# Optimization experiments

Hardware: AMD Instinct MI355X
Metric: run time of the kernel (lower is better)

## Reference

```python
import jax, jax.numpy as jnp
import numpy as np

B, N, D, H = 4, 4096, 1024, 16
DH = D // H          # per-head dim = 64
M = 256              # number of random features
KEPS = 1e-3          # performer kernel epsilon
LNEPS = 1e-5


def setup_inputs() -> dict:
    key = jax.random.key(0)
    ks = jax.random.split(key, 16)
    s = 0.02
    return {
        "src": jax.random.normal(ks[0], (B, N, D), jnp.float32),
        "Wq": s * jax.random.normal(ks[1], (D, D), jnp.float32),
        "Wk": s * jax.random.normal(ks[2], (D, D), jnp.float32),
        "Wv": s * jax.random.normal(ks[3], (D, D), jnp.float32),
        "Wout": s * jax.random.normal(ks[4], (D, D), jnp.float32),
        "b_out": jnp.zeros((D,), jnp.float32),
        "proj": jax.random.normal(ks[5], (M, DH), jnp.float32),
        "g1": jnp.ones((D,), jnp.float32),
        "beta1": jnp.zeros((D,), jnp.float32),
        "W1": s * jax.random.normal(ks[6], (2048, D), jnp.float32),
        "b1": jnp.zeros((2048,), jnp.float32),
        "W2": s * jax.random.normal(ks[7], (D, 2048), jnp.float32),
        "b2": jnp.zeros((D,), jnp.float32),
        "g2": jnp.ones((D,), jnp.float32),
        "beta2": jnp.zeros((D,), jnp.float32),
    }


def _layernorm(x, g, b):
    mu = x.mean(-1, keepdims=True)
    var = ((x - mu) ** 2).mean(-1, keepdims=True)
    return (x - mu) * jax.lax.rsqrt(var + LNEPS) * g + b


def _softmax_kernel(x, proj, is_query):
    # FAVOR+ positive softmax kernel feature map (performer_pytorch)
    dn = DH ** -0.25           # data normalizer d^{-1/4}
    ratio = M ** -0.5
    data_dash = jnp.einsum('bhnd,md->bhnm', x * dn, proj)
    diag = (x ** 2).sum(-1) * 0.5 * dn * dn            # [b,h,n]
    if is_query:
        stab = data_dash.max(-1, keepdims=True)
    else:
        stab = data_dash.max()
    return ratio * (jnp.exp(data_dash - diag[..., None] - stab) + KEPS)


def reference(src, Wq, Wk, Wv, Wout, b_out, proj, g1, beta1, W1, b1, W2, b2, g2, beta2):
    # ---- Performer self-attention (FAVOR+, non-causal) ----
    def split_heads(x):
        return x.reshape(B, N, H, DH).transpose(0, 2, 1, 3)  # [b,h,n,dh]

    q = split_heads(src @ Wq.T)
    k = split_heads(src @ Wk.T)
    v = split_heads(src @ Wv.T)

    qp = _softmax_kernel(q, proj, is_query=True)   # [b,h,n,m]
    kp = _softmax_kernel(k, proj, is_query=False)  # [b,h,n,m]

    k_sum = kp.sum(-2)                                        # [b,h,m]
    d_inv = 1.0 / jnp.einsum('bhnm,bhm->bhn', qp, k_sum)      # [b,h,n]
    context = jnp.einsum('bhnm,bhnd->bhmd', kp, v)            # [b,h,m,dh]
    attn = jnp.einsum('bhnm,bhmd->bhnd', qp, context) * d_inv[..., None]

    attn = attn.transpose(0, 2, 1, 3).reshape(B, N, D)
    src2 = attn @ Wout.T + b_out

    # ---- residual + norm + FFN (dropout = identity at eval) ----
    x = _layernorm(src + src2, g1, beta1)
    ff = (jax.nn.gelu(x @ W1.T + b1, approximate=False)) @ W2.T + b2
    return _layernorm(x + ff, g2, beta2)
```

## Files before the change

kernel.cpp:

```cpp
#include <hip/hip_runtime.h>

#define DEVI __device__ __forceinline__

using u16 = unsigned short;
using u32 = unsigned int;
using u64 = unsigned long long;

typedef __bf16 bf16x8 __attribute__((ext_vector_type(8)));
typedef __bf16 bf16x4 __attribute__((ext_vector_type(4)));
typedef float  f32x4  __attribute__((ext_vector_type(4)));

constexpr int BB = 4, NN = 4096, DD = 1024, HH = 16, DH = 64, MF = 256;
constexpr int RT = BB * NN;
constexpr int QKVS = 3072;
constexpr float DN    = 0.35355339059327373f;
constexpr float RATIO = 0.0625f;
constexpr float DIAGC = 0.0625f;
constexpr float KEPSC = 1e-3f;

DEVI u16 f2bf(float f) {
  u32 u = __float_as_uint(f);
  u32 r = u + 0x7fffu + ((u >> 16) & 1u);
  return (u16)(r >> 16);
}
DEVI float bf2f(u16 u) { return __uint_as_float(((u32)u) << 16); }

typedef void __attribute__((address_space(1)))* gas1;
typedef void __attribute__((address_space(3)))* las3;
DEVI void gload_lds16(const void* g, void* l) {
  __builtin_amdgcn_global_load_lds((gas1)(u64)g, (las3)(u32)(u64)l, 16, 0, 0);
}

DEVI bf16x8 ldswz(const u16* base, int row, int kbyte) {
  int p = (row << 7) + kbyte;
  p ^= (row & 7) << 4;
  return *(const bf16x8*)((const char*)base + p);
}

__global__ void cast_kernel(const float* __restrict__ in, u16* __restrict__ out, int n4) {
  int i = blockIdx.x * 256 + threadIdx.x;
  int stride = gridDim.x * 256;
  for (; i < n4; i += stride) {
    float4 v = ((const float4*)in)[i];
    ushort4 o; o.x = f2bf(v.x); o.y = f2bf(v.y); o.z = f2bf(v.z); o.w = f2bf(v.w);
    ((ushort4*)out)[i] = o;
  }
}

__global__ void cast_weights_kernel(
    const float* __restrict__ Wq, const float* __restrict__ Wk,
    const float* __restrict__ Wv, const float* __restrict__ Wout,
    const float* __restrict__ W1, const float* __restrict__ W2,
    const float* __restrict__ proj,
    u16* __restrict__ wqkvb, u16* __restrict__ wob,
    u16* __restrict__ w1b, u16* __restrict__ w2b, u16* __restrict__ projb)
{
  constexpr int TOT = 2101248;
  int i = blockIdx.x * 256 + threadIdx.x;
  const int stride = gridDim.x * 256;
  for (; i < TOT; i += stride) {
    const float* s; u16* d; int loc; float sc = 1.0f;
    if (i < 1048576) {
      int seg = i >> 18; loc = i & 262143;
      s = (seg == 0) ? Wq : (seg == 1) ? Wk : (seg == 2) ? Wv : Wout;
      d = (seg < 3) ? (wqkvb + seg * 1048576) : wob;
    } else if (i < 1572864) { loc = i - 1048576; s = W1; d = w1b; }
    else if (i < 2097152)   { loc = i - 1572864; s = W2; d = w2b; }
    else                    { loc = i - 2097152; s = proj; d = projb; sc = DN; }
    float4 v = ((const float4*)s)[loc];
    ushort4 o; o.x = f2bf(v.x * sc); o.y = f2bf(v.y * sc); o.z = f2bf(v.z * sc); o.w = f2bf(v.w * sc);
    ((ushort4*)d)[loc] = o;
  }
}

template <int EPI>
__global__ __launch_bounds__(256, 2) void gemm_bt(
    const u16* __restrict__ A, int lda, const u16* __restrict__ Bm,
    u16* __restrict__ Cb, const float* __restrict__ bias,
    int Ncols, int K)
{
  __shared__ __align__(16) u16 sA[128 * 64];
  __shared__ __align__(16) u16 sB[128 * 64];
  const int tid = threadIdx.x, lane = tid & 63;
  const int wv = tid >> 6, wr = wv >> 1, wc = wv & 1;

  const int gx = gridDim.x;
  const int wg = blockIdx.y * gx + blockIdx.x;
  const int cpx = (gx * gridDim.y) >> 3;
  const int swz = (wg & 7) * cpx + (wg >> 3);
  const int bn = swz % gx, bm = swz / gx;

  f32x4 acc[4][4] = {};

  int rowS[4], colS[4], ldsb[4];
#pragma unroll
  for (int it = 0; it < 4; ++it) {
    int p = (it * 256 + tid) * 16;
    ldsb[it] = (it * 256 + (tid & ~63)) * 16;
    int sp = p ^ (((p >> 7) & 7) << 4);
    rowS[it] = sp >> 7;
    colS[it] = (sp >> 1) & 63;
  }
  const size_t baseA = (size_t)bm * 128, baseB = (size_t)bn * 128;

  for (int kt = 0; kt < K; kt += 64) {
#pragma unroll
    for (int it = 0; it < 4; ++it)
      gload_lds16(A + (baseA + rowS[it]) * lda + kt + colS[it], (char*)sA + ldsb[it]);
#pragma unroll
    for (int it = 0; it < 4; ++it)
      gload_lds16(Bm + (baseB + rowS[it]) * K + kt + colS[it], (char*)sB + ldsb[it]);
    __syncthreads();
#pragma unroll
    for (int kk = 0; kk < 2; ++kk) {
      const int kbyte = kk * 64 + ((lane >> 4) << 4);
      bf16x8 a[4], b[4];
#pragma unroll
      for (int i = 0; i < 4; ++i) a[i] = ldswz(sA, wr * 64 + i * 16 + (lane & 15), kbyte);
#pragma unroll
      for (int i = 0; i < 4; ++i) b[i] = ldswz(sB, wc * 64 + i * 16 + (lane & 15), kbyte);
#pragma unroll
      for (int i = 0; i < 4; ++i)
#pragma unroll
        for (int j = 0; j < 4; ++j)
          acc[i][j] = __builtin_amdgcn_mfma_f32_16x16x32_bf16(a[i], b[j], acc[i][j], 0, 0, 0);
    }
    __syncthreads();
  }

#pragma unroll
  for (int i = 0; i < 4; ++i) {
    const int gr0 = bm * 128 + wr * 64 + i * 16 + ((lane >> 4) << 2);
#pragma unroll
    for (int j = 0; j < 4; ++j) {
      const int gc = bn * 128 + wc * 64 + j * 16 + (lane & 15);
#pragma unroll
      for (int r = 0; r < 4; ++r) {
        const size_t o = (size_t)(gr0 + r) * Ncols + gc;
        const float v = acc[i][j][r];
        if constexpr (EPI == 0) {
          Cb[o] = f2bf(v);
        } else if constexpr (EPI == 2) {
          float t = v + bias[gc];
          Cb[o] = f2bf(0.5f * t * (1.0f + erff(t * 0.70710678118654752f)));
        } else {
          Cb[o] = f2bf(v + bias[gc]);
        }
      }
    }
  }
}

__global__ __launch_bounds__(256) void kmax_kernel(
    const u16* __restrict__ qkvb, const u16* __restrict__ projb, float* __restrict__ pmax)
{
  __shared__ __align__(16) u16 sX[64 * 72];
  __shared__ float sred[4];
  const int tid = threadIdx.x, lane = tid & 63, wv = tid >> 6;
  const int bh = blockIdx.x, b = bh >> 4, h = bh & 15;
  const int n0 = blockIdx.y * 64;

  for (int i = tid; i < 512; i += 256) {
    int r = i >> 3, c8 = (i & 7) << 3;
    uint4 v = *(const uint4*)(qkvb + ((size_t)(b * NN + n0 + r)) * QKVS + 1024 + h * DH + c8);
    *(uint4*)&sX[r * 72 + c8] = v;
  }
  __syncthreads();

  f32x4 dacc[16] = {};
#pragma unroll
  for (int kk = 0; kk < 2; ++kk) {
    const int ko = kk * 32 + ((lane >> 4) << 3);
    bf16x8 a = *(const bf16x8*)&sX[(wv * 16 + (lane & 15)) * 72 + ko];
#pragma unroll
    for (int f = 0; f < 16; ++f) {
      bf16x8 bb = *(const bf16x8*)(projb + (f * 16 + (lane & 15)) * 64 + ko);
      dacc[f] = __builtin_amdgcn_mfma_f32_16x16x32_bf16(a, bb, dacc[f], 0, 0, 0);
    }
  }
  float mx = -1e30f;
#pragma unroll
  for (int f = 0; f < 16; ++f)
#pragma unroll
    for (int r = 0; r < 4; ++r) mx = fmaxf(mx, dacc[f][r]);
#pragma unroll
  for (int m = 1; m < 64; m <<= 1) mx = fmaxf(mx, __shfl_xor(mx, m));
  if (lane == 0) sred[wv] = mx;
  __syncthreads();
  if (tid == 0)
    pmax[blockIdx.y * gridDim.x + blockIdx.x] =
        fmaxf(fmaxf(sred[0], sred[1]), fmaxf(sred[2], sred[3]));
}

__global__ __launch_bounds__(256) void reduce_max_kernel(
    const float* __restrict__ pmax, float* __restrict__ stab)
{
  const int tid = threadIdx.x;
  float mx = -1e30f;
#pragma unroll
  for (int i = 0; i < 16; ++i) mx = fmaxf(mx, pmax[i * 256 + tid]);
#pragma unroll
  for (int m = 1; m < 64; m <<= 1) mx = fmaxf(mx, __shfl_xor(mx, m));
  __shared__ float sred[4];
  if ((tid & 63) == 0) sred[tid >> 6] = mx;
  __syncthreads();
  if (tid == 0)
    stab[0] = fmaxf(fmaxf(sred[0], sred[1]), fmaxf(sred[2], sred[3]));
}

__global__ __launch_bounds__(512, 4) void kctx_kernel(
    const u16* __restrict__ qkvb, const u16* __restrict__ projb,
    const float* __restrict__ stab_p,
    float* __restrict__ ctxP, float* __restrict__ ksum)
{
  __shared__ __align__(16) u16 sX[64 * 72];
  __shared__ __align__(16) u16 sVT[64 * 68];
  __shared__ __align__(16) u16 sKpT[256 * 72];
  __shared__ float sDiag[64];
  const int tid = threadIdx.x, lane = tid & 63, wv = tid >> 6;
  const int nw = wv & 3;
  const int mh = wv >> 2;
  const int bh = blockIdx.x, b = bh >> 4, h = bh & 15;
  const int sl = blockIdx.y;
  const float stab = stab_p[0];

  f32x4 cacc[8] = {};
  float ksacc[8] = {};
  const int row_base = nw * 16 + ((lane >> 4) << 2);

  for (int t = 0; t < 8; ++t) {
    const int n0 = sl * 512 + t * 64;
    if (t) __syncthreads();
    {
      int r = tid >> 3, c8 = (tid & 7) << 3;
      size_t g = ((size_t)(b * NN + n0 + r)) * QKVS + h * DH + c8;
      uint4 xv = *(const uint4*)(qkvb + g + 1024);
      *(uint4*)&sX[r * 72 + c8] = xv;
      {
        const u16* px = (const u16*)&xv;
        float s = 0;
#pragma unroll
        for (int j = 0; j < 8; ++j) { float x = bf2f(px[j]); s += x * x; }
        s += __shfl_xor(s, 1); s += __shfl_xor(s, 2); s += __shfl_xor(s, 4);
        if ((tid & 7) == 0) sDiag[r] = DIAGC * s;
      }
      uint4 vv = *(const uint4*)(qkvb + g + 2048);
      const u16* pv = (const u16*)&vv;
#pragma unroll
      for (int j = 0; j < 8; ++j) sVT[(c8 + j) * 68 + r] = pv[j];
    }
    __syncthreads();

    f32x4 dacc[8] = {};
#pragma unroll
    for (int kk = 0; kk < 2; ++kk) {
      const int ko = kk * 32 + ((lane >> 4) << 3);
      bf16x8 a = *(const bf16x8*)&sX[(nw * 16 + (lane & 15)) * 72 + ko];
#pragma unroll
      for (int f = 0; f < 8; ++f) {
        bf16x8 bb = *(const bf16x8*)(projb + (mh * 128 + f * 16 + (lane & 15)) * 64 + ko);
        dacc[f] = __builtin_amdgcn_mfma_f32_16x16x32_bf16(a, bb, dacc[f], 0, 0, 0);
      }
    }
#pragma unroll
    for (int f = 0; f < 8; ++f) {
      float kvv[4]; float cs = 0;
#pragma unroll
      for (int r = 0; r < 4; ++r) {
        float val = RATIO * (__expf(dacc[f][r] - sDiag[row_base + r] - stab) + KEPSC);
        kvv[r] = val; cs += val;
      }
      cs += __shfl_xor(cs, 16); cs += __shfl_xor(cs, 32);
      ksacc[f] += cs;
      ushort4 pk; pk.x = f2bf(kvv[0]); pk.y = f2bf(kvv[1]); pk.z = f2bf(kvv[2]); pk.w = f2bf(kvv[3]);
      *(ushort4*)&sKpT[(mh * 128 + f * 16 + (lane & 15)) * 72 + row_base] = pk;
    }
    __syncthreads();
#pragma unroll
    for (int kk = 0; kk < 2; ++kk) {
      const int ko = kk * 32 + ((lane >> 4) << 3);
      const int vrow = nw * 16 + (lane & 15);
      bf16x4 lo = *(const bf16x4*)&sVT[vrow * 68 + ko];
      bf16x4 hi = *(const bf16x4*)&sVT[vrow * 68 + ko + 4];
      bf16x8 a;
#pragma unroll
      for (int e = 0; e < 4; ++e) { a[e] = lo[e]; a[e + 4] = hi[e]; }
#pragma unroll
      for (int f = 0; f < 8; ++f) {
        bf16x8 bb = *(const bf16x8*)&sKpT[(mh * 128 + f * 16 + (lane & 15)) * 72 + ko];
        cacc[f] = __builtin_amdgcn_mfma_f32_16x16x32_bf16(a, bb, cacc[f], 0, 0, 0);
      }
    }
  }
  float* cp = ctxP + (size_t)(sl * 64 + bh) * 16384;
#pragma unroll
  for (int f = 0; f < 8; ++f) {
    const int m = mh * 128 + f * 16 + (lane & 15);
#pragma unroll
    for (int r = 0; r < 4; ++r)
      cp[(row_base + r) * 256 + m] = cacc[f][r];
  }
  if (lane < 16) {
#pragma unroll
    for (int f = 0; f < 8; ++f)
      atomicAdd(&ksum[bh * 256 + mh * 128 + f * 16 + lane], ksacc[f]);
  }
}

__global__ __launch_bounds__(256) void ctxfin_kernel(
    const float* __restrict__ ctxP, u16* __restrict__ ctxb)
{
  const int idx = blockIdx.x * 256 + threadIdx.x;
  const int bh = idx >> 12, pos = idx & 4095;
  float4 s = {0, 0, 0, 0};
#pragma unroll
  for (int sl = 0; sl < 8; ++sl) {
    float4 v = *(const float4*)(ctxP + (size_t)(sl * 64 + bh) * 16384 + pos * 4);
    s.x += v.x; s.y += v.y; s.z += v.z; s.w += v.w;
  }
  ushort4 o; o.x = f2bf(s.x); o.y = f2bf(s.y); o.z = f2bf(s.z); o.w = f2bf(s.w);
  *(ushort4*)(ctxb + (size_t)bh * 16384 + pos * 4) = o;
}

__global__ __launch_bounds__(256, 2) void qattn_kernel(
    u16* qkvb, const u16* __restrict__ projb,
    const u16* __restrict__ ctxb, const float* __restrict__ ksum)
{
  __shared__ __align__(16) u16 sCtx[64 * 256];
  __shared__ __align__(16) u16 sX[64 * 72];
  __shared__ __align__(16) u16 sQp[64 * 264];
  __shared__ float sKsum[256];
  __shared__ float sDiag[64];
  __shared__ float sDinv[64];
  const int tid = threadIdx.x, lane = tid & 63, wv = tid >> 6;
  const int bh = blockIdx.x, b = bh >> 4, h = bh & 15;

  {
    const char* cbase = (const char*)(ctxb + (size_t)bh * 16384);
#pragma unroll
    for (int it = 0; it < 8; ++it) {
      int p = (it * 256 + tid) * 16;
      int ldsb = (it * 256 + (tid & ~63)) * 16;
      int q = p ^ (((p >> 9) & 7) << 4);
      gload_lds16(cbase + q, (char*)sCtx + ldsb);
    }
  }
  sKsum[tid] = ksum[bh * 256 + tid];

  const int row_base = wv * 16 + ((lane >> 4) << 2);
  const int wr = wv >> 1, wc = wv & 1;

  for (int rt = 0; rt < 2; ++rt) {
    const int n0 = (blockIdx.y * 2 + rt) * 64;
    for (int i = tid; i < 512; i += 256) {
      int r = i >> 3, c8 = (i & 7) << 3;
      uint4 v = *(const uint4*)(qkvb + ((size_t)(b * NN + n0 + r)) * QKVS + h * DH + c8);
      *(uint4*)&sX[r * 72 + c8] = v;
    }
    __syncthreads();
    {
      int r = tid >> 2, qq = tid & 3;
      float s = 0;
#pragma unroll
      for (int j = 0; j < 16; ++j) { float x = bf2f(sX[r * 72 + qq * 16 + j]); s += x * x; }
      s += __shfl_xor(s, 1); s += __shfl_xor(s, 2);
      if (qq == 0) sDiag[r] = DIAGC * s;
    }
    f32x4 dacc[16] = {};
#pragma unroll
    for (int kk = 0; kk < 2; ++kk) {
      const int ko = kk * 32 + ((lane >> 4) << 3);
      bf16x8 a = *(const bf16x8*)&sX[(wv * 16 + (lane & 15)) * 72 + ko];
#pragma unroll
      for (int f = 0; f < 16; ++f) {
        bf16x8 bb = *(const bf16x8*)(projb + (f * 16 + (lane & 15)) * 64 + ko);
        dacc[f] = __builtin_amdgcn_mfma_f32_16x16x32_bf16(a, bb, dacc[f], 0, 0, 0);
      }
    }
    __syncthreads();
#pragma unroll
    for (int r = 0; r < 4; ++r) {
      const int row = row_base + r;
      float mx = dacc[0][r];
#pragma unroll
      for (int f = 1; f < 16; ++f) mx = fmaxf(mx, dacc[f][r]);
      mx = fmaxf(mx, __shfl_xor(mx, 1));
      mx = fmaxf(mx, __shfl_xor(mx, 2));
      mx = fmaxf(mx, __shfl_xor(mx, 4));
      mx = fmaxf(mx, __shfl_xor(mx, 8));
      const float dg = sDiag[row];
      float ds = 0;
#pragma unroll
      for (int f = 0; f < 16; ++f) {
        float qv = RATIO * (__expf(dacc[f][r] - dg - mx) + KEPSC);
        dacc[f][r] = qv;
        ds += qv * sKsum[f * 16 + (lane & 15)];
      }
      ds += __shfl_xor(ds, 1); ds += __shfl_xor(ds, 2);
      ds += __shfl_xor(ds, 4); ds += __shfl_xor(ds, 8);
      if ((lane & 15) == 0) sDinv[row] = 1.0f / ds;
    }
#pragma unroll
    for (int f = 0; f < 16; ++f)
#pragma unroll
      for (int r = 0; r < 4; ++r)
        sQp[(row_base + r) * 264 + f * 16 + (lane & 15)] = f2bf(dacc[f][r]);
    __syncthreads();

    f32x4 acc2[2][2] = {};
#pragma unroll
    for (int kk = 0; kk < 8; ++kk) {
      const int koe = kk * 32 + ((lane >> 4) << 3);
      const int kob = koe * 2;
      bf16x8 a0 = *(const bf16x8*)&sQp[(wr * 32 + (lane & 15)) * 264 + koe];
      bf16x8 a1 = *(const bf16x8*)&sQp[(wr * 32 + 16 + (lane & 15)) * 264 + koe];
      const int j0 = wc * 32 + (lane & 15), j1 = j0 + 16;
      bf16x8 b0 = *(const bf16x8*)((const char*)sCtx + (((j0 << 9) + kob) ^ ((j0 & 7) << 4)));
      bf16x8 b1 = *(const bf16x8*)((const char*)sCtx + (((j1 << 9) + kob) ^ ((j1 & 7) << 4)));
      acc2[0][0] = __builtin_amdgcn_mfma_f32_16x16x32_bf16(a0, b0, acc2[0][0], 0, 0, 0);
      acc2[0][1] = __builtin_amdgcn_mfma_f32_16x16x32_bf16(a0, b1, acc2[0][1], 0, 0, 0);
      acc2[1][0] = __builtin_amdgcn_mfma_f32_16x16x32_bf16(a1, b0, acc2[1][0], 0, 0, 0);
      acc2[1][1] = __builtin_amdgcn_mfma_f32_16x16x32_bf16(a1, b1, acc2[1][1], 0, 0, 0);
    }
#pragma unroll
    for (int mi = 0; mi < 2; ++mi)
#pragma unroll
      for (int ni = 0; ni < 2; ++ni)
#pragma unroll
        for (int r = 0; r < 4; ++r) {
          const int row = wr * 32 + mi * 16 + ((lane >> 4) << 2) + r;
          const int col = wc * 32 + ni * 16 + (lane & 15);
          float v = acc2[mi][ni][r] * sDinv[row];
          qkvb[((size_t)(b * NN + n0 + row)) * QKVS + h * DH + col] = f2bf(v);
        }
    __syncthreads();
  }
}

__global__ __launch_bounds__(256) void ln1_kernel(
    const float* __restrict__ src, const u16* __restrict__ wout,
    const float* __restrict__ g, const float* __restrict__ be, u16* __restrict__ xb)
{
  const int row = blockIdx.x, tid = threadIdx.x;
  const float4 sv = ((const float4*)(src + (size_t)row * DD))[tid];
  const ushort4 wv = ((const ushort4*)(wout + (size_t)row * DD))[tid];
  float x0 = sv.x + bf2f(wv.x);
  float x1 = sv.y + bf2f(wv.y);
  float x2 = sv.z + bf2f(wv.z);
  float x3 = sv.w + bf2f(wv.w);
  float s = x0 + x1 + x2 + x3;
  float ss = x0 * x0 + x1 * x1 + x2 * x2 + x3 * x3;
#pragma unroll
  for (int m = 1; m < 64; m <<= 1) { s += __shfl_xor(s, m); ss += __shfl_xor(ss, m); }
  __shared__ float red[8];
  if ((tid & 63) == 0) { red[tid >> 6] = s; red[4 + (tid >> 6)] = ss; }
  __syncthreads();
  s = red[0] + red[1] + red[2] + red[3];
  ss = red[4] + red[5] + red[6] + red[7];
  const float mu = s * (1.0f / DD);
  const float rs = rsqrtf(ss * (1.0f / DD) - mu * mu + 1e-5f);
  const float4 gv = ((const float4*)g)[tid];
  const float4 bv = ((const float4*)be)[tid];
  ushort4 o;
  o.x = f2bf((x0 - mu) * rs * gv.x + bv.x);
  o.y = f2bf((x1 - mu) * rs * gv.y + bv.y);
  o.z = f2bf((x2 - mu) * rs * gv.z + bv.z);
  o.w = f2bf((x3 - mu) * rs * gv.w + bv.w);
  ((ushort4*)(xb + (size_t)row * DD))[tid] = o;
}

__global__ __launch_bounds__(256) void ln2_kernel(
    const u16* __restrict__ xb, const u16* __restrict__ ff,
    const float* __restrict__ g, const float* __restrict__ be, float* __restrict__ out)
{
  const int row = blockIdx.x, tid = threadIdx.x;
  const ushort4 xv = ((const ushort4*)(xb + (size_t)row * DD))[tid];
  const ushort4 fv = ((const ushort4*)(ff + (size_t)row * DD))[tid];
  float x0 = bf2f(xv.x) + bf2f(fv.x);
  float x1 = bf2f(xv.y) + bf2f(fv.y);
  float x2 = bf2f(xv.z) + bf2f(fv.z);
  float x3 = bf2f(xv.w) + bf2f(fv.w);
  float s = x0 + x1 + x2 + x3;
  float ss = x0 * x0 + x1 * x1 + x2 * x2 + x3 * x3;
#pragma unroll
  for (int m = 1; m < 64; m <<= 1) { s += __shfl_xor(s, m); ss += __shfl_xor(ss, m); }
  __shared__ float red[8];
  if ((tid & 63) == 0) { red[tid >> 6] = s; red[4 + (tid >> 6)] = ss; }
  __syncthreads();
  s = red[0] + red[1] + red[2] + red[3];
  ss = red[4] + red[5] + red[6] + red[7];
  const float mu = s * (1.0f / DD);
  const float rs = rsqrtf(ss * (1.0f / DD) - mu * mu + 1e-5f);
  const float4 gv = ((const float4*)g)[tid];
  const float4 bv = ((const float4*)be)[tid];
  float4 o;
  o.x = (x0 - mu) * rs * gv.x + bv.x;
  o.y = (x1 - mu) * rs * gv.y + bv.y;
  o.z = (x2 - mu) * rs * gv.z + bv.z;
  o.w = (x3 - mu) * rs * gv.w + bv.w;
  ((float4*)(out + (size_t)row * DD))[tid] = o;
}

extern "C" void kernel_launch(void* const* d_in, const int* in_sizes, int n_in,
                              void* d_out, int out_size, void* d_ws, size_t ws_size,
                              hipStream_t stream) {
  (void)in_sizes; (void)n_in; (void)out_size; (void)ws_size;
  const float* src   = (const float*)d_in[0];
  const float* Wq    = (const float*)d_in[1];
  const float* Wk    = (const float*)d_in[2];
  const float* Wv    = (const float*)d_in[3];
  const float* Wout  = (const float*)d_in[4];
  const float* b_out = (const float*)d_in[5];
  const float* proj  = (const float*)d_in[6];
  const float* g1    = (const float*)d_in[7];
  const float* be1   = (const float*)d_in[8];
  const float* W1    = (const float*)d_in[9];
  const float* b1    = (const float*)d_in[10];
  const float* W2    = (const float*)d_in[11];
  const float* b2    = (const float*)d_in[12];
  const float* g2    = (const float*)d_in[13];
  const float* be2   = (const float*)d_in[14];

  char* ws = (char*)d_ws;
  constexpr size_t OFF_SRCB = 0;
  constexpr size_t OFF_QKV  = 33554432;
  constexpr size_t OFF_XB   = 67108864;
  constexpr size_t OFF_WOUTB= 100663296;
  constexpr size_t OFF_WQKV = 134217728;
  constexpr size_t OFF_WO   = 140509184;
  constexpr size_t OFF_W1   = 142606336;
  constexpr size_t OFF_W2   = 146800640;
  constexpr size_t OFF_PROJ = 150994944;
  constexpr size_t OFF_CTXB = 151027712;
  constexpr size_t OFF_KSUM = 153124864;
  constexpr size_t OFF_PMAX = 153190400;
  constexpr size_t OFF_STAB = 153206784;

  u16* srcb  = (u16*)(ws + OFF_SRCB);
  u16* qkvb  = (u16*)(ws + OFF_QKV);
  u16* wqkvb = (u16*)(ws + OFF_WQKV);
  u16* wob   = (u16*)(ws + OFF_WO);
  u16* w1b   = (u16*)(ws + OFF_W1);
  u16* w2b   = (u16*)(ws + OFF_W2);
  u16* projb = (u16*)(ws + OFF_PROJ);
  u16* ctxb  = (u16*)(ws + OFF_CTXB);
  float* ksum = (float*)(ws + OFF_KSUM);
  float* pmax = (float*)(ws + OFF_PMAX);
  float* stab = (float*)(ws + OFF_STAB);
  float* ctxP = (float*)(ws + OFF_SRCB);
  u16* woutb = (u16*)(ws + OFF_WOUTB);
  u16* xb    = (u16*)(ws + OFF_XB);
  u16* h1    = (u16*)(ws + OFF_SRCB);
  u16* ff    = (u16*)(ws + OFF_WOUTB);

  cast_kernel<<<4096, 256, 0, stream>>>(src, srcb, RT * DD / 4);
  cast_weights_kernel<<<2048, 256, 0, stream>>>(Wq, Wk, Wv, Wout, W1, W2, proj,
                                                wqkvb, wob, w1b, w2b, projb);
  hipMemsetAsync(ws + OFF_KSUM, 0, 65536, stream);

  gemm_bt<0><<<dim3(QKVS / 128, RT / 128), 256, 0, stream>>>(srcb, DD, wqkvb, qkvb, nullptr, QKVS, DD);

  kmax_kernel<<<dim3(64, 64), 256, 0, stream>>>(qkvb, projb, pmax);
  reduce_max_kernel<<<1, 256, 0, stream>>>(pmax, stab);
  kctx_kernel<<<dim3(64, 8), 512, 0, stream>>>(qkvb, projb, stab, ctxP, ksum);
  ctxfin_kernel<<<1024, 256, 0, stream>>>(ctxP, ctxb);
  qattn_kernel<<<dim3(64, 32), 256, 0, stream>>>(qkvb, projb, ctxb, ksum);

  gemm_bt<3><<<dim3(DD / 128, RT / 128), 256, 0, stream>>>(qkvb, QKVS, wob, woutb, b_out, DD, DD);
  ln1_kernel<<<RT, 256, 0, stream>>>(src, woutb, g1, be1, xb);

  gemm_bt<2><<<dim3(2048 / 128, RT / 128), 256, 0, stream>>>(xb, DD, w1b, h1, b1, 2048, DD);
  gemm_bt<3><<<dim3(DD / 128, RT / 128), 256, 0, stream>>>(h1, 2048, w2b, ff, b2, DD, 2048);
  ln2_kernel<<<RT, 256, 0, stream>>>(xb, ff, g2, be2, (float*)d_out);
}
```

Measured before the change: 779.1 us.

## Replace ksum atomics with partials, drop GEMM tile swizzle, enlarge qattn row tiles

The kctx kernel now writes per-wave ksum partials to a scratch buffer instead of using atomicAdd, and the ctxfin kernel gains extra blocks that reduce those partials, so the memset is no longer needed. Separately, the GEMM drops its workgroup swizzle in favour of plain blockIdx mapping, and qattn processes four row tiles per block instead of two, with half the grid. These cut atomic traffic and a launch and amortize the ctx load in qattn, but removing the swizzle may hurt L2 reuse in the large GEMMs.

```diff
diff --git a/kernel.cpp b/kernel.cpp
--- a/kernel.cpp
+++ b/kernel.cpp
@@ -83,12 +83,7 @@
   __shared__ __align__(16) u16 sB[128 * 64];
   const int tid = threadIdx.x, lane = tid & 63;
   const int wv = tid >> 6, wr = wv >> 1, wc = wv & 1;
-
-  const int gx = gridDim.x;
-  const int wg = blockIdx.y * gx + blockIdx.x;
-  const int cpx = (gx * gridDim.y) >> 3;
-  const int swz = (wg & 7) * cpx + (wg >> 3);
-  const int bn = swz % gx, bm = swz / gx;
+  const int bm = blockIdx.y, bn = blockIdx.x;
 
   f32x4 acc[4][4] = {};
 
@@ -211,7 +206,7 @@
 __global__ __launch_bounds__(512, 4) void kctx_kernel(
     const u16* __restrict__ qkvb, const u16* __restrict__ projb,
     const float* __restrict__ stab_p,
-    float* __restrict__ ctxP, float* __restrict__ ksum)
+    float* __restrict__ ctxP, float* __restrict__ ksumP)
 {
   __shared__ __align__(16) u16 sX[64 * 72];
   __shared__ __align__(16) u16 sVT[64 * 68];
@@ -301,25 +296,40 @@
       cp[(row_base + r) * 256 + m] = cacc[f][r];
   }
   if (lane < 16) {
-#pragma unroll
-    for (int f = 0; f < 8; ++f)
-      atomicAdd(&ksum[bh * 256 + mh * 128 + f * 16 + lane], ksacc[f]);
+    float* kp = ksumP + ((size_t)(sl * 64 + bh) * 8 + wv) * 128;
+#pragma unroll
+    for (int f = 0; f < 8; ++f) kp[f * 16 + lane] = ksacc[f];
   }
 }
 
 __global__ __launch_bounds__(256) void ctxfin_kernel(
-    const float* __restrict__ ctxP, u16* __restrict__ ctxb)
-{
-  const int idx = blockIdx.x * 256 + threadIdx.x;
-  const int bh = idx >> 12, pos = idx & 4095;
-  float4 s = {0, 0, 0, 0};
-#pragma unroll
-  for (int sl = 0; sl < 8; ++sl) {
-    float4 v = *(const float4*)(ctxP + (size_t)(sl * 64 + bh) * 16384 + pos * 4);
-    s.x += v.x; s.y += v.y; s.z += v.z; s.w += v.w;
-  }
-  ushort4 o; o.x = f2bf(s.x); o.y = f2bf(s.y); o.z = f2bf(s.z); o.w = f2bf(s.w);
-  *(ushort4*)(ctxb + (size_t)bh * 16384 + pos * 4) = o;
+    const float* __restrict__ ctxP, const float* __restrict__ ksumP,
+    u16* __restrict__ ctxb, float* __restrict__ ksum)
+{
+  const int bid = blockIdx.x, tid = threadIdx.x;
+  if (bid < 1024) {
+    const int idx = bid * 256 + tid;
+    const int bh = idx >> 12, pos = idx & 4095;
+    float4 s = {0, 0, 0, 0};
+#pragma unroll
+    for (int sl = 0; sl < 8; ++sl) {
+      float4 v = *(const float4*)(ctxP + (size_t)(sl * 64 + bh) * 16384 + pos * 4);
+      s.x += v.x; s.y += v.y; s.z += v.z; s.w += v.w;
+    }
+    ushort4 o; o.x = f2bf(s.x); o.y = f2bf(s.y); o.z = f2bf(s.z); o.w = f2bf(s.w);
+    *(ushort4*)(ctxb + (size_t)bh * 16384 + pos * 4) = o;
+  } else {
+    const int idx = (bid - 1024) * 256 + tid;
+    const int bh = idx >> 8, m = idx & 255;
+    const int mh = m >> 7, ml = m & 127;
+    float s = 0;
+#pragma unroll
+    for (int sl = 0; sl < 8; ++sl)
+#pragma unroll
+      for (int nw = 0; nw < 4; ++nw)
+        s += ksumP[((size_t)(sl * 64 + bh) * 8 + mh * 4 + nw) * 128 + ml];
+    ksum[idx] = s;
+  }
 }
 
 __global__ __launch_bounds__(256, 2) void qattn_kernel(
@@ -350,8 +360,8 @@
   const int row_base = wv * 16 + ((lane >> 4) << 2);
   const int wr = wv >> 1, wc = wv & 1;
 
-  for (int rt = 0; rt < 2; ++rt) {
-    const int n0 = (blockIdx.y * 2 + rt) * 64;
+  for (int rt = 0; rt < 4; ++rt) {
+    const int n0 = (blockIdx.y * 4 + rt) * 64;
     for (int i = tid; i < 512; i += 256) {
       int r = i >> 3, c8 = (i & 7) << 3;
       uint4 v = *(const uint4*)(qkvb + ((size_t)(b * NN + n0 + r)) * QKVS + h * DH + c8);
@@ -533,8 +543,9 @@
   constexpr size_t OFF_PROJ = 150994944;
   constexpr size_t OFF_CTXB = 151027712;
   constexpr size_t OFF_KSUM = 153124864;
-  constexpr size_t OFF_PMAX = 153190400;
-  constexpr size_t OFF_STAB = 153206784;
+  constexpr size_t OFF_KSP  = 153190400;
+  constexpr size_t OFF_PMAX = 155287552;
+  constexpr size_t OFF_STAB = 155303936;
 
   u16* srcb  = (u16*)(ws + OFF_SRCB);
   u16* qkvb  = (u16*)(ws + OFF_QKV);
@@ -544,9 +555,10 @@
   u16* w2b   = (u16*)(ws + OFF_W2);
   u16* projb = (u16*)(ws + OFF_PROJ);
   u16* ctxb  = (u16*)(ws + OFF_CTXB);
-  float* ksum = (float*)(ws + OFF_KSUM);
-  float* pmax = (float*)(ws + OFF_PMAX);
-  float* stab = (float*)(ws + OFF_STAB);
+  float* ksum  = (float*)(ws + OFF_KSUM);
+  float* ksumP = (float*)(ws + OFF_KSP);
+  float* pmax  = (float*)(ws + OFF_PMAX);
+  float* stab  = (float*)(ws + OFF_STAB);
   float* ctxP = (float*)(ws + OFF_SRCB);
   u16* woutb = (u16*)(ws + OFF_WOUTB);
   u16* xb    = (u16*)(ws + OFF_XB);
@@ -556,15 +568,14 @@
   cast_kernel<<<4096, 256, 0, stream>>>(src, srcb, RT * DD / 4);
   cast_weights_kernel<<<2048, 256, 0, stream>>>(Wq, Wk, Wv, Wout, W1, W2, proj,
                                                 wqkvb, wob, w1b, w2b, projb);
-  hipMemsetAsync(ws + OFF_KSUM, 0, 65536, stream);
 
   gemm_bt<0><<<dim3(QKVS / 128, RT / 128), 256, 0, stream>>>(srcb, DD, wqkvb, qkvb, nullptr, QKVS, DD);
 
   kmax_kernel<<<dim3(64, 64), 256, 0, stream>>>(qkvb, projb, pmax);
   reduce_max_kernel<<<1, 256, 0, stream>>>(pmax, stab);
-  kctx_kernel<<<dim3(64, 8), 512, 0, stream>>>(qkvb, projb, stab, ctxP, ksum);
-  ctxfin_kernel<<<1024, 256, 0, stream>>>(ctxP, ctxb);
-  qattn_kernel<<<dim3(64, 32), 256, 0, stream>>>(qkvb, projb, ctxb, ksum);
+  kctx_kernel<<<dim3(64, 8), 512, 0, stream>>>(qkvb, projb, stab, ctxP, ksumP);
+  ctxfin_kernel<<<1088, 256, 0, stream>>>(ctxP, ksumP, ctxb, ksum);
+  qattn_kernel<<<dim3(64, 16), 256, 0, stream>>>(qkvb, projb, ctxb, ksum);
 
   gemm_bt<3><<<dim3(DD / 128, RT / 128), 256, 0, stream>>>(qkvb, QKVS, wob, woutb, b_out, DD, DD);
   ln1_kernel<<<RT, 256, 0, stream>>>(src, woutb, g1, be1, xb);
```

New measurement: 794.5 us. Within noise of the previous version (+2.0%).
